# Kernel optimization log

Measured on AMD Instinct MI355X. Metric: run time of the kernel, lower is better.

Reference implementation:

```python
import math
import jax, jax.numpy as jnp
import numpy as np

HEADS = 16
MASKED_BIAS = -10000.0


def setup_inputs() -> dict:
    key = jax.random.key(0)
    kq, kk, kv = jax.random.split(key, 3)
    B, S, D = 4, 1024, 2048
    q = jax.random.normal(kq, (B, S, D), dtype=jnp.float32)
    k = jax.random.normal(kk, (B, S, D), dtype=jnp.float32)
    v = jax.random.normal(kv, (B, S, D), dtype=jnp.float32)
    return {"q": q, "k": k, "v": v}


def _mha(q, k, v):
    B, Sq, D = q.shape
    Sk = k.shape[-2]
    hd = D // HEADS
    # (B, H, S, hd)
    qh = q.reshape(B, Sq, HEADS, hd).transpose(0, 2, 1, 3)
    kh = k.reshape(B, Sk, HEADS, hd).transpose(0, 2, 1, 3)
    vh = v.reshape(B, Sk, HEADS, hd).transpose(0, 2, 1, 3)
    scores = jnp.einsum("bhqd,bhkd->bhqk", qh, kh) / math.sqrt(hd)
    # causal mask: query i attends to keys <= i (aligned to end of kv)
    qi = jnp.arange(Sq)[:, None] + (Sk - Sq)
    ki = jnp.arange(Sk)[None, :]
    causal = ki <= qi  # (Sq, Sk)
    scores = jnp.where(causal[None, None], scores, jnp.asarray(MASKED_BIAS, scores.dtype))
    attn = jax.nn.softmax(scores, axis=-1)
    out = jnp.einsum("bhqk,bhkd->bhqd", attn, vh)
    return out.transpose(0, 2, 1, 3).reshape(B, Sq, D)


def reference(q, k, v):
    return _mha(q, k, v)
```

## Files before the change

kernel.cpp:

```cpp
#include <hip/hip_runtime.h>
#include <hip/hip_bf16.h>


#define HEADS  16
#define HD     128
#define SEQ    1024
#define DMODEL 2048
#define IMG_CHUNK 32768

typedef _Float16 f16;
typedef __attribute__((ext_vector_type(8))) _Float16 f16x8;
typedef __attribute__((ext_vector_type(4))) _Float16 f16x4;
typedef __attribute__((ext_vector_type(4))) float    f32x4;
typedef __attribute__((ext_vector_type(4))) unsigned int u32x4;

typedef __attribute__((address_space(1))) const unsigned char gl_u8;
typedef __attribute__((address_space(3))) unsigned char lds_u8;

__device__ unsigned char KVIMG[64ull * 16ull * IMG_CHUNK];

__device__ __forceinline__ unsigned int pkrtz(float a, float b) {
    return __builtin_bit_cast(unsigned int, __builtin_amdgcn_cvt_pkrtz(a, b));
}

__device__ __forceinline__ void dma16(const void* g, void* l) {
    __builtin_amdgcn_global_load_lds((gl_u8*)g, (lds_u8*)l, 16, 0, 0);
}

__global__ __launch_bounds__(256, 2)
void prep_kv(const float* __restrict__ K, const float* __restrict__ V)
{
    __shared__ f16 kL[64 * 128];
    __shared__ f16 vL[128 * 64];

    const int tid = threadIdx.x;
    const int bh  = blockIdx.x;
    const int kb  = blockIdx.y;
    const long long head_off = ((long long)(bh >> 4) * SEQ) * DMODEL
                             + (long long)(bh & 15) * HD;
    const int kbase = kb * 64;

    const int krow = tid >> 4;
    const int kg   = tid & 15;
    const int kgs  = kg ^ krow;
    #pragma unroll
    for (int i = 0; i < 4; ++i) {
        const float* kp = K + head_off + (long long)(kbase + krow + 16 * i) * DMODEL + kg * 8;
        f32x4 a = *(const f32x4*)kp;
        f32x4 b = *(const f32x4*)(kp + 4);
        u32x4 w;
        w.x = pkrtz(a[0], a[1]); w.y = pkrtz(a[2], a[3]);
        w.z = pkrtz(b[0], b[1]); w.w = pkrtz(b[2], b[3]);
        *(u32x4*)&kL[(krow + 16 * i) * 128 + kgs * 8] = w;
    }
    const int vr0 = (tid & 31) * 2;
    const int vcg = tid >> 5;
    const int vg  = vr0 >> 3;
    const int vo  = vr0 & 7;
    {
        const float* vp = V + head_off + (long long)(kbase + vr0) * DMODEL + vcg * 16;
        f32x4 va[4], vb[4];
        #pragma unroll
        for (int j = 0; j < 4; ++j) {
            va[j] = *(const f32x4*)(vp + 4 * j);
            vb[j] = *(const f32x4*)(vp + DMODEL + 4 * j);
        }
        #pragma unroll
        for (int j = 0; j < 16; ++j) {
            unsigned int pk = pkrtz(va[j >> 2][j & 3], vb[j >> 2][j & 3]);
            *(unsigned int*)&vL[(vcg * 16 + j) * 64 + ((vg ^ (j & 7)) * 8) + vo] = pk;
        }
    }
    __syncthreads();

    unsigned char* dst = KVIMG + ((long long)(bh * 16 + kb)) * IMG_CHUNK;
    const unsigned char* ks = (const unsigned char*)kL;
    const unsigned char* vs = (const unsigned char*)vL;
    #pragma unroll
    for (int i = 0; i < 4; ++i) {
        *(u32x4*)(dst + tid * 16 + i * 4096)         = *(const u32x4*)(ks + tid * 16 + i * 4096);
        *(u32x4*)(dst + 16384 + tid * 16 + i * 4096) = *(const u32x4*)(vs + tid * 16 + i * 4096);
    }
}

__global__ __launch_bounds__(256, 2)
void fa_fwd(const float* __restrict__ Q, float* __restrict__ O)
{
    __shared__ f16 kT[2][64 * 128];
    __shared__ f16 vT[2][128 * 64];

    const int tid  = threadIdx.x;
    const int lane = tid & 63;
    const int wv   = tid >> 6;
    const int quad = lane >> 4;
    const int cl   = lane & 15;

    const int bh = blockIdx.x;
    const int qt = 15 - blockIdx.y;
    const int qb = qt * 64;
    const long long head_off = ((long long)(bh >> 4) * SEQ) * DMODEL
                             + (long long)(bh & 15) * HD;
    const float rscale = 0.08838834764831845f;

    const unsigned char* img = KVIMG + (long long)bh * 16 * IMG_CHUNK;

    auto issueTile = [&](int buf, int kt) {
        const unsigned char* src = img + (long long)kt * IMG_CHUNK + wv * 4096 + lane * 16;
        unsigned char* kb = (unsigned char*)&kT[buf][0] + wv * 4096;
        unsigned char* vb = (unsigned char*)&vT[buf][0] + wv * 4096;
        #pragma unroll
        for (int i = 0; i < 4; ++i) dma16(src + i * 1024,          kb + i * 1024);
        #pragma unroll
        for (int i = 0; i < 4; ++i) dma16(src + 16384 + i * 1024,  vb + i * 1024);
    };

    const int qrow = qb + wv * 16 + cl;
    f16x8 qf[4];
    {
        const float* qp = Q + head_off + (long long)qrow * DMODEL + quad * 8;
        #pragma unroll
        for (int kk = 0; kk < 4; ++kk) {
            f32x4 qa = *(const f32x4*)(qp + kk * 32);
            f32x4 qc = *(const f32x4*)(qp + kk * 32 + 4);
            union { f16x8 v; unsigned int u[4]; } qw;
            qw.u[0] = pkrtz(qa[0], qa[1]);
            qw.u[1] = pkrtz(qa[2], qa[3]);
            qw.u[2] = pkrtz(qc[0], qc[1]);
            qw.u[3] = pkrtz(qc[2], qc[3]);
            qf[kk] = qw.v;
        }
    }

    f32x4 acc[8];
    #pragma unroll
    for (int i = 0; i < 8; ++i) acc[i] = (f32x4){0.f, 0.f, 0.f, 0.f};
    float ls = 0.f;

    issueTile(0, 0);

    #pragma unroll 1
    for (int kt = 0; kt <= qt; ++kt) {
        const int c = kt & 1;

        __syncthreads();

        if (kt < qt) issueTile(c ^ 1, kt + 1);

        f32x4 sc[4];
        #pragma unroll
        for (int st = 0; st < 4; ++st) sc[st] = (f32x4){0.f, 0.f, 0.f, 0.f};
        __builtin_amdgcn_s_setprio(1);
        #pragma unroll
        for (int kk = 0; kk < 4; ++kk) {
            #pragma unroll
            for (int st = 0; st < 4; ++st) {
                f16x8 kf = *(const f16x8*)&kT[c][(st * 16 + cl) * 128
                                               + ((kk * 4 + quad) ^ cl) * 8];
                sc[st] = __builtin_amdgcn_mfma_f32_16x16x32_f16(kf, qf[kk], sc[st], 0, 0, 0);
            }
        }
        __builtin_amdgcn_s_setprio(0);

        const int kbase = kt * 64;
        f16x4 pf[4];
        if (kt == qt) {
            #pragma unroll
            for (int st = 0; st < 4; ++st) {
                float e[4];
                #pragma unroll
                for (int r = 0; r < 4; ++r) {
                    int key = kbase + st * 16 + quad * 4 + r;
                    float ex = __expf(sc[st][r] * rscale);
                    e[r] = (key <= qrow) ? ex : 0.f;
                    ls += e[r];
                }
                union { f16x4 v; unsigned int u[2]; } pw;
                pw.u[0] = pkrtz(e[0], e[1]);
                pw.u[1] = pkrtz(e[2], e[3]);
                pf[st] = pw.v;
            }
        } else {
            #pragma unroll
            for (int st = 0; st < 4; ++st) {
                float e[4];
                #pragma unroll
                for (int r = 0; r < 4; ++r) {
                    e[r] = __expf(sc[st][r] * rscale);
                    ls += e[r];
                }
                union { f16x4 v; unsigned int u[2]; } pw;
                pw.u[0] = pkrtz(e[0], e[1]);
                pw.u[1] = pkrtz(e[2], e[3]);
                pf[st] = pw.v;
            }
        }

        __builtin_amdgcn_s_setprio(1);
        #pragma unroll
        for (int dt = 0; dt < 8; ++dt) {
            #pragma unroll
            for (int st = 0; st < 4; ++st) {
                f16x4 vf = *(const f16x4*)&vT[c][(dt * 16 + cl) * 64
                                                + ((st * 2 + (quad >> 1)) ^ (cl & 7)) * 8
                                                + (quad & 1) * 4];
                acc[dt] = __builtin_amdgcn_mfma_f32_16x16x16f16(vf, pf[st], acc[dt], 0, 0, 0);
            }
        }
        __builtin_amdgcn_s_setprio(0);
    }

    float lsum = ls;
    lsum += __shfl_xor(lsum, 16, 64);
    lsum += __shfl_xor(lsum, 32, 64);
    const float rl = 1.0f / lsum;

    float* op = O + head_off + (long long)qrow * DMODEL + quad * 4;
    #pragma unroll
    for (int dt = 0; dt < 8; ++dt) {
        f32x4 o4 = acc[dt];
        o4[0] *= rl; o4[1] *= rl; o4[2] *= rl; o4[3] *= rl;
        *(f32x4*)(op + dt * 16) = o4;
    }
}

extern "C" void kernel_launch(void* const* d_in, const int* in_sizes, int n_in,
                              void* d_out, int out_size, void* d_ws, size_t ws_size,
                              hipStream_t stream) {
    const float* q = (const float*)d_in[0];
    const float* k = (const float*)d_in[1];
    const float* v = (const float*)d_in[2];
    float* o = (float*)d_out;

    prep_kv<<<dim3(64, 16), dim3(256), 0, stream>>>(k, v);
    fa_fwd <<<dim3(64, 16), dim3(256), 0, stream>>>(q, o);
}
```

Before: 174.2 us.

## Single-buffer K/V LDS with staggered loads; write prep output directly to global

The attention kernel goes from double-buffered K and V tiles to single K and V buffers. V for the current tile is loaded while QK^T runs, and K for the next tile is loaded while PV runs, with an extra barrier per iteration. This halves LDS use per block so launch bounds can allow 4 blocks per CU for more occupancy. The prep kernel now writes the swizzled fp16 K/V image straight to global memory instead of staging it in LDS, dropping a barrier and a copy at the cost of less coalesced V stores.

After: 171.7 us. No clear change (-1.4%).

```diff
diff --git a/kernel.cpp b/kernel.cpp
--- a/kernel.cpp
+++ b/kernel.cpp
@@ -27,31 +27,30 @@
     __builtin_amdgcn_global_load_lds((gl_u8*)g, (lds_u8*)l, 16, 0, 0);
 }
 
-__global__ __launch_bounds__(256, 2)
+__global__ __launch_bounds__(256)
 void prep_kv(const float* __restrict__ K, const float* __restrict__ V)
 {
-    __shared__ f16 kL[64 * 128];
-    __shared__ f16 vL[128 * 64];
-
     const int tid = threadIdx.x;
     const int bh  = blockIdx.x;
     const int kb  = blockIdx.y;
     const long long head_off = ((long long)(bh >> 4) * SEQ) * DMODEL
                              + (long long)(bh & 15) * HD;
     const int kbase = kb * 64;
+    unsigned char* dst = KVIMG + ((long long)(bh * 16 + kb)) * IMG_CHUNK;
 
     const int krow = tid >> 4;
     const int kg   = tid & 15;
     const int kgs  = kg ^ krow;
     #pragma unroll
     for (int i = 0; i < 4; ++i) {
-        const float* kp = K + head_off + (long long)(kbase + krow + 16 * i) * DMODEL + kg * 8;
+        const int row = krow + 16 * i;
+        const float* kp = K + head_off + (long long)(kbase + row) * DMODEL + kg * 8;
         f32x4 a = *(const f32x4*)kp;
         f32x4 b = *(const f32x4*)(kp + 4);
         u32x4 w;
         w.x = pkrtz(a[0], a[1]); w.y = pkrtz(a[2], a[3]);
         w.z = pkrtz(b[0], b[1]); w.w = pkrtz(b[2], b[3]);
-        *(u32x4*)&kL[(krow + 16 * i) * 128 + kgs * 8] = w;
+        *(u32x4*)(dst + row * 256 + kgs * 16) = w;
     }
     const int vr0 = (tid & 31) * 2;
     const int vcg = tid >> 5;
@@ -67,27 +66,18 @@
         }
         #pragma unroll
         for (int j = 0; j < 16; ++j) {
+            const int d = vcg * 16 + j;
             unsigned int pk = pkrtz(va[j >> 2][j & 3], vb[j >> 2][j & 3]);
-            *(unsigned int*)&vL[(vcg * 16 + j) * 64 + ((vg ^ (j & 7)) * 8) + vo] = pk;
-        }
-    }
-    __syncthreads();
-
-    unsigned char* dst = KVIMG + ((long long)(bh * 16 + kb)) * IMG_CHUNK;
-    const unsigned char* ks = (const unsigned char*)kL;
-    const unsigned char* vs = (const unsigned char*)vL;
-    #pragma unroll
-    for (int i = 0; i < 4; ++i) {
-        *(u32x4*)(dst + tid * 16 + i * 4096)         = *(const u32x4*)(ks + tid * 16 + i * 4096);
-        *(u32x4*)(dst + 16384 + tid * 16 + i * 4096) = *(const u32x4*)(vs + tid * 16 + i * 4096);
-    }
-}
-
-__global__ __launch_bounds__(256, 2)
+            *(unsigned int*)(dst + 16384 + (d * 64 + ((vg ^ (j & 7)) * 8) + vo) * 2) = pk;
+        }
+    }
+}
+
+__global__ __launch_bounds__(256, 4)
 void fa_fwd(const float* __restrict__ Q, float* __restrict__ O)
 {
-    __shared__ f16 kT[2][64 * 128];
-    __shared__ f16 vT[2][128 * 64];
+    __shared__ f16 kT[64 * 128];
+    __shared__ f16 vT[128 * 64];
 
     const int tid  = threadIdx.x;
     const int lane = tid & 63;
@@ -104,14 +94,17 @@
 
     const unsigned char* img = KVIMG + (long long)bh * 16 * IMG_CHUNK;
 
-    auto issueTile = [&](int buf, int kt) {
+    auto issueK = [&](int kt) {
         const unsigned char* src = img + (long long)kt * IMG_CHUNK + wv * 4096 + lane * 16;
-        unsigned char* kb = (unsigned char*)&kT[buf][0] + wv * 4096;
-        unsigned char* vb = (unsigned char*)&vT[buf][0] + wv * 4096;
-        #pragma unroll
-        for (int i = 0; i < 4; ++i) dma16(src + i * 1024,          kb + i * 1024);
-        #pragma unroll
-        for (int i = 0; i < 4; ++i) dma16(src + 16384 + i * 1024,  vb + i * 1024);
+        unsigned char* d = (unsigned char*)&kT[0] + wv * 4096;
+        #pragma unroll
+        for (int i = 0; i < 4; ++i) dma16(src + i * 1024, d + i * 1024);
+    };
+    auto issueV = [&](int kt) {
+        const unsigned char* src = img + (long long)kt * IMG_CHUNK + 16384 + wv * 4096 + lane * 16;
+        unsigned char* d = (unsigned char*)&vT[0] + wv * 4096;
+        #pragma unroll
+        for (int i = 0; i < 4; ++i) dma16(src + i * 1024, d + i * 1024);
     };
 
     const int qrow = qb + wv * 16 + cl;
@@ -136,15 +129,13 @@
     for (int i = 0; i < 8; ++i) acc[i] = (f32x4){0.f, 0.f, 0.f, 0.f};
     float ls = 0.f;
 
-    issueTile(0, 0);
+    issueK(0);
 
     #pragma unroll 1
     for (int kt = 0; kt <= qt; ++kt) {
-        const int c = kt & 1;
-
         __syncthreads();
 
-        if (kt < qt) issueTile(c ^ 1, kt + 1);
+        issueV(kt);
 
         f32x4 sc[4];
         #pragma unroll
@@ -154,8 +145,8 @@
         for (int kk = 0; kk < 4; ++kk) {
             #pragma unroll
             for (int st = 0; st < 4; ++st) {
-                f16x8 kf = *(const f16x8*)&kT[c][(st * 16 + cl) * 128
-                                               + ((kk * 4 + quad) ^ cl) * 8];
+                f16x8 kf = *(const f16x8*)&kT[(st * 16 + cl) * 128
+                                              + ((kk * 4 + quad) ^ cl) * 8];
                 sc[st] = __builtin_amdgcn_mfma_f32_16x16x32_f16(kf, qf[kk], sc[st], 0, 0, 0);
             }
         }
@@ -195,14 +186,18 @@
             }
         }
 
+        __syncthreads();
+
+        if (kt < qt) issueK(kt + 1);
+
         __builtin_amdgcn_s_setprio(1);
         #pragma unroll
         for (int dt = 0; dt < 8; ++dt) {
             #pragma unroll
             for (int st = 0; st < 4; ++st) {
-                f16x4 vf = *(const f16x4*)&vT[c][(dt * 16 + cl) * 64
-                                                + ((st * 2 + (quad >> 1)) ^ (cl & 7)) * 8
-                                                + (quad & 1) * 4];
+                f16x4 vf = *(const f16x4*)&vT[(dt * 16 + cl) * 64
+                                              + ((st * 2 + (quad >> 1)) ^ (cl & 7)) * 8
+                                              + (quad & 1) * 4];
                 acc[dt] = __builtin_amdgcn_mfma_f32_16x16x16f16(vf, pf[st], acc[dt], 0, 0, 0);
             }
         }
```
